# Kernel tuning notes

Hardware: AMD Instinct MI355X
Metric: run time of the kernel (lower is better)

Reference implementation:

```python
import jax, jax.numpy as jnp
import numpy as np

ROW, COL = 135, 240          # input_size / ratio
N = ROW * COL                # 32400 sampled pixels
MB = 2025                    # minibatch_size
NITER = N // MB              # 16
K = 9                        # feature_neibor_length
NC = 19                      # num_classes
FULL_ROW, FULL_COL = 1080, 1920
H, W, C = 270, 480, 512


def setup_inputs() -> dict:
    key = jax.random.key(0)
    k1, k2, k3, k4 = jax.random.split(key, 4)
    features_tensor = jax.random.normal(k1, (1, C, H, W), jnp.float32)
    outputs = jax.random.normal(k2, (1, NC, H, W), jnp.float32)
    classes_prototypes = jax.random.normal(k3, (1, NC, C), jnp.float32)
    # random.sample -> unique indices, then sorted (torch.sort on sampled ids)
    sample_index = jnp.sort(jax.random.permutation(k4, H * W)[:N]).astype(jnp.int32)
    return {"features_tensor": features_tensor, "outputs": outputs,
            "classes_prototypes": classes_prototypes, "sample_index": sample_index}


def reference(features_tensor, outputs, classes_prototypes, sample_index):
    b, c, h, w = features_tensor.shape
    # [1,C,H,W] -> [H*W,C], gather sampled pixels -> [N,C]
    feats = features_tensor[0].transpose(1, 2, 0).reshape(h * w, c)[sample_index]
    # predicted class per pixel (softmax is monotone -> argmax over class dim)
    cls = jnp.argmax(outputs[0].reshape(NC, h * w), axis=0)[sample_index]  # [N] int
    protos = classes_prototypes[0]                       # [NC, C]
    feats_sq = jnp.sum(feats * feats, axis=-1)           # [N]
    proto_sq = jnp.sum(protos * protos, axis=-1)         # [NC]

    def step(_, xs):
        mb_feats, mb_cls = xs                            # [MB,C], [MB]
        mb_sq = jnp.sum(mb_feats * mb_feats, axis=-1)    # [MB]
        # squared Euclidean distance, clamped (dim==3 branch: no sqrt)
        d = mb_sq[:, None] - 2.0 * (mb_feats @ feats.T) + feats_sq[None, :]
        d = jnp.maximum(d, 1e-12)                        # [MB, N]
        _, idx = jax.lax.top_k(-d, K)                    # K nearest -> [MB, K]
        nb_cls = cls[idx]                                # neighbor class ids [MB,K]
        counts = jnp.sum(jax.nn.one_hot(nb_cls, NC, dtype=jnp.float32), axis=1)  # [MB,NC]
        p = counts / float(K)
        ent = jnp.sum(-p * jnp.log(p + 1e-6), axis=1) / np.float32(np.log(NC))   # [MB]
        # disparity: rank of predicted class among prototypes sorted by distance
        dp = mb_sq[:, None] - 2.0 * (mb_feats @ protos.T) + proto_sq[None, :]
        dp = jnp.maximum(dp, 1e-12)                      # [MB, NC]
        order = jnp.argsort(dp, axis=1)                  # [MB, NC] class ids by distance
        rank = jnp.argmax(order == mb_cls[:, None], axis=1)  # [MB]
        score = rank.astype(jnp.float32) / float(NC - 1)
        return None, (ent, score)

    xs = (feats.reshape(NITER, MB, c), cls.reshape(NITER, MB))
    _, (ents, scores) = jax.lax.scan(step, None, xs)
    purity = ents.reshape(N)
    entropy = scores.reshape(N)
    full_p = jnp.zeros(FULL_ROW * FULL_COL, jnp.float32).at[sample_index].set(purity)
    full_e = jnp.zeros(FULL_ROW * FULL_COL, jnp.float32).at[sample_index].set(entropy)
    return (full_p.reshape(FULL_ROW, FULL_COL), full_e.reshape(FULL_ROW, FULL_COL))
```

## Files before the change

### kernel.cpp

```cpp
#include <hip/hip_runtime.h>
#include <math.h>

#define H_ 270
#define W_ 480
#define HW_ (H_ * W_)
#define C_ 512
#define NC_ 19
#define N_ 32400
#define NP_ 32512
#define FULLPIX 2073600
#define K_ 9

#define BM 64
#define BN 128
#define BK 16
#define TM 4
#define TN 8

static_assert(NP_ % BN == 0, "pad");
static_assert(NP_ % BM == 0, "pad");
static_assert(C_ % BK == 0, "pad");

__global__ void gather_kernel(const float* __restrict__ feat,
                              const int* __restrict__ sidx,
                              float* __restrict__ MT) {
    int i = blockIdx.x * 256 + threadIdx.x;
    int c = blockIdx.y;
    float v = 0.0f;
    if (i < N_) v = feat[(size_t)c * HW_ + sidx[i]];
    MT[(size_t)c * NP_ + i] = v;
}

__global__ void sq_kernel(const float* __restrict__ MT, float* __restrict__ fsq) {
    int i = blockIdx.x * 256 + threadIdx.x;
    float s = 0.0f;
    for (int c = 0; c < C_; ++c) {
        float v = MT[(size_t)c * NP_ + i];
        s = fmaf(v, v, s);
    }
    fsq[i] = (i < N_) ? s : 1e30f;
}

__global__ void cls_kernel(const float* __restrict__ outs,
                           const int* __restrict__ sidx,
                           int* __restrict__ cls) {
    int i = blockIdx.x * 256 + threadIdx.x;
    if (i >= NP_) return;
    if (i >= N_) { cls[i] = 0; return; }
    int p = sidx[i];
    float best = outs[p];
    int bk = 0;
#pragma unroll
    for (int k = 1; k < NC_; ++k) {
        float v = outs[(size_t)k * HW_ + p];
        if (v > best) { best = v; bk = k; }
    }
    cls[i] = bk;
}

__launch_bounds__(256, 2)
__global__ void knn_kernel(const float* __restrict__ MT,
                           const float* __restrict__ fsq,
                           const int* __restrict__ cls,
                           const int* __restrict__ sidx,
                           float* __restrict__ out) {
    __shared__ float As[BK][BM];
    __shared__ float Bs[BK][BN];
    __shared__ float dT[BN][BM + 4];

    const int tid = threadIdx.x;
    const int tx = tid & 15;
    const int ty = tid >> 4;
    const int ibase = blockIdx.x * BM;

    float t9d[K_];
    int   t9i[K_];
#pragma unroll
    for (int s = 0; s < K_; ++s) { t9d[s] = 1e38f; t9i[s] = -1; }
    float w9 = 1e38f;

    float si[TM];
#pragma unroll
    for (int m = 0; m < TM; ++m) si[m] = fsq[ibase + ty * TM + m];

    float acc[TM][TN];

    for (int jt = 0; jt < NP_ / BN; ++jt) {
        const int jbase = jt * BN;
#pragma unroll
        for (int m = 0; m < TM; ++m)
#pragma unroll
            for (int n = 0; n < TN; ++n) acc[m][n] = 0.0f;

        for (int ck = 0; ck < C_ / BK; ++ck) {
            const int cc = ck * BK;
            {
                int kk = tid >> 4, seg = tid & 15;
                *(float4*)&As[kk][seg * 4] =
                    *(const float4*)&MT[(size_t)(cc + kk) * NP_ + ibase + seg * 4];
            }
#pragma unroll
            for (int l = 0; l < 2; ++l) {
                int idx = tid + l * 256;
                int kk = idx >> 5, seg = idx & 31;
                *(float4*)&Bs[kk][seg * 4] =
                    *(const float4*)&MT[(size_t)(cc + kk) * NP_ + jbase + seg * 4];
            }
            __syncthreads();
#pragma unroll
            for (int kk = 0; kk < BK; ++kk) {
                float4 av  = *(const float4*)&As[kk][ty * TM];
                float4 bv0 = *(const float4*)&Bs[kk][tx * TN];
                float4 bv1 = *(const float4*)&Bs[kk][tx * TN + 4];
                float a[TM] = {av.x, av.y, av.z, av.w};
                float b[TN] = {bv0.x, bv0.y, bv0.z, bv0.w, bv1.x, bv1.y, bv1.z, bv1.w};
#pragma unroll
                for (int m = 0; m < TM; ++m)
#pragma unroll
                    for (int n = 0; n < TN; ++n)
                        acc[m][n] = fmaf(a[m], b[n], acc[m][n]);
            }
            __syncthreads();
        }

        float sj[TN];
#pragma unroll
        for (int n = 0; n < TN; ++n) sj[n] = fsq[jbase + tx * TN + n];
#pragma unroll
        for (int n = 0; n < TN; ++n) {
            float d0 = fmaxf(si[0] - 2.0f * acc[0][n] + sj[n], 1e-12f);
            float d1 = fmaxf(si[1] - 2.0f * acc[1][n] + sj[n], 1e-12f);
            float d2 = fmaxf(si[2] - 2.0f * acc[2][n] + sj[n], 1e-12f);
            float d3 = fmaxf(si[3] - 2.0f * acc[3][n] + sj[n], 1e-12f);
            *(float4*)&dT[tx * TN + n][ty * TM] = make_float4(d0, d1, d2, d3);
        }
        __syncthreads();

        if (tid < BM) {
            int jlim = min(BN, N_ - jbase);
#pragma unroll 4
            for (int jj = 0; jj < jlim; ++jj) {
                float d = dT[jj][tid];
                if (d < w9) {
                    float cd = d;
                    int   ci = jbase + jj;
#pragma unroll
                    for (int s = 0; s < K_; ++s) {
                        if (cd < t9d[s]) {
                            float td = t9d[s]; t9d[s] = cd; cd = td;
                            int   ti = t9i[s]; t9i[s] = ci; ci = ti;
                        }
                    }
                    w9 = t9d[K_ - 1];
                }
            }
        }
    }

    if (tid < BM) {
        int i = ibase + tid;
        if (i < N_) {
            int nb[K_];
#pragma unroll
            for (int s = 0; s < K_; ++s) nb[s] = cls[t9i[s]];
            float ent = 0.0f;
#pragma unroll
            for (int k = 0; k < NC_; ++k) {
                int c = 0;
#pragma unroll
                for (int s = 0; s < K_; ++s) c += (nb[s] == k) ? 1 : 0;
                if (c > 0) {
                    float p = (float)c / 9.0f;
                    ent += -p * logf(p + 1e-6f);
                }
            }
            ent = ent / 2.9444389791664403f;
            out[sidx[i]] = ent;
        }
    }
}

__global__ void proto_kernel(const float* __restrict__ MT,
                             const float* __restrict__ fsq,
                             const int* __restrict__ cls,
                             const int* __restrict__ sidx,
                             const float* __restrict__ protos,
                             float* __restrict__ out) {
    __shared__ float P[NC_][C_];
    __shared__ float psq[NC_];
    int tid = threadIdx.x;
    for (int idx = tid; idx < NC_ * C_; idx += 256)
        P[idx >> 9][idx & (C_ - 1)] = protos[idx];
    __syncthreads();
    if (tid < NC_) {
        float s = 0.0f;
        for (int c = 0; c < C_; ++c) { float v = P[tid][c]; s = fmaf(v, v, s); }
        psq[tid] = s;
    }
    __syncthreads();

    int i = blockIdx.x * 256 + tid;
    if (i >= N_) return;

    float accp[NC_];
#pragma unroll
    for (int k = 0; k < NC_; ++k) accp[k] = 0.0f;
    for (int c = 0; c < C_; ++c) {
        float f = MT[(size_t)c * NP_ + i];
#pragma unroll
        for (int k = 0; k < NC_; ++k) accp[k] = fmaf(f, P[k][c], accp[k]);
    }
    float s = fsq[i];
    int ci = cls[i];
    float dp[NC_];
    float dc = 0.0f;
#pragma unroll
    for (int k = 0; k < NC_; ++k) {
        float v = fmaxf(s - 2.0f * accp[k] + psq[k], 1e-12f);
        dp[k] = v;
        if (k == ci) dc = v;
    }
    int rank = 0;
#pragma unroll
    for (int k = 0; k < NC_; ++k) {
        rank += (dp[k] < dc) ? 1 : 0;
        rank += ((k < ci) && (dp[k] == dc)) ? 1 : 0;
    }
    out[FULLPIX + sidx[i]] = (float)rank / 18.0f;
}

extern "C" void kernel_launch(void* const* d_in, const int* in_sizes, int n_in,
                              void* d_out, int out_size, void* d_ws, size_t ws_size,
                              hipStream_t stream) {
    const float* feat   = (const float*)d_in[0];
    const float* outs   = (const float*)d_in[1];
    const float* protos = (const float*)d_in[2];
    const int*   sidx   = (const int*)d_in[3];
    float* out = (float*)d_out;

    char* ws = (char*)d_ws;
    float* MT  = (float*)ws;
    float* fsq = (float*)(ws + (size_t)66584576);
    int*   cls = (int*)(ws + (size_t)66584576 + 130048);

    hipMemsetAsync(d_out, 0, (size_t)2 * FULLPIX * sizeof(float), stream);

    gather_kernel<<<dim3(NP_ / 256, C_), 256, 0, stream>>>(feat, sidx, MT);
    sq_kernel<<<NP_ / 256, 256, 0, stream>>>(MT, fsq);
    cls_kernel<<<NP_ / 256, 256, 0, stream>>>(outs, sidx, cls);
    knn_kernel<<<NP_ / BM, 256, 0, stream>>>(MT, fsq, cls, sidx, out);
    proto_kernel<<<NP_ / 256, 256, 0, stream>>>(MT, fsq, cls, sidx, protos, out);
}
```

Measured before the change: 23.31 ms.

## Split KNN column range across blocks, distribute top-k selection, double-buffer GEMM tiles

Splits the candidate dimension into four parts so that four times as many blocks run, and adds a finalize kernel that merges the per-part top-9 lists and computes the entropy. Every thread now keeps its own top-9 for two rows across 16 columns, and the lists are merged through shared memory. Before, only 64 threads per block did the serial insertion. The GEMM loop gains register-staged double buffering and XOR-swizzled B tiles to cut bank conflicts. The row norm and the clamp are dropped from the comparison because they do not change the ordering. The cost is extra workspace traffic for the partial results, more registers per thread, and tie-breaking by index that may differ slightly from top_k.

```diff
diff --git a/kernel.cpp b/kernel.cpp
--- a/kernel.cpp
+++ b/kernel.cpp
@@ -14,8 +14,10 @@
 #define BM 64
 #define BN 128
 #define BK 16
-#define TM 4
-#define TN 8
+#define NTILES (NP_ / BN)
+#define CKS (C_ / BK)
+#define JSPLIT 4
+#define TILES_PER_PART 64
 
 static_assert(NP_ % BN == 0, "pad");
 static_assert(NP_ % BM == 0, "pad");
@@ -58,126 +60,207 @@
     cls[i] = bk;
 }
 
-__launch_bounds__(256, 2)
+union SmU {
+    struct { float As[2][BK][BM]; float Bs[2][BK * BN]; } st;
+    struct { float md[BM][73]; int mi[BM][73]; } mg;
+};
+
+#define FMA4(bv, n0)                                                        \
+    acc[0][(n0) + 0] = fmaf(av.x, (bv).x, acc[0][(n0) + 0]);                \
+    acc[1][(n0) + 0] = fmaf(av.y, (bv).x, acc[1][(n0) + 0]);                \
+    acc[0][(n0) + 1] = fmaf(av.x, (bv).y, acc[0][(n0) + 1]);                \
+    acc[1][(n0) + 1] = fmaf(av.y, (bv).y, acc[1][(n0) + 1]);                \
+    acc[0][(n0) + 2] = fmaf(av.x, (bv).z, acc[0][(n0) + 2]);                \
+    acc[1][(n0) + 2] = fmaf(av.y, (bv).z, acc[1][(n0) + 2]);                \
+    acc[0][(n0) + 3] = fmaf(av.x, (bv).w, acc[0][(n0) + 3]);                \
+    acc[1][(n0) + 3] = fmaf(av.y, (bv).w, acc[1][(n0) + 3]);
+
+__launch_bounds__(256, 3)
 __global__ void knn_kernel(const float* __restrict__ MT,
                            const float* __restrict__ fsq,
-                           const int* __restrict__ cls,
-                           const int* __restrict__ sidx,
-                           float* __restrict__ out) {
-    __shared__ float As[BK][BM];
-    __shared__ float Bs[BK][BN];
-    __shared__ float dT[BN][BM + 4];
-
-    const int tid = threadIdx.x;
-    const int tx = tid & 15;
-    const int ty = tid >> 4;
-    const int ibase = blockIdx.x * BM;
-
-    float t9d[K_];
-    int   t9i[K_];
-#pragma unroll
-    for (int s = 0; s < K_; ++s) { t9d[s] = 1e38f; t9i[s] = -1; }
-    float w9 = 1e38f;
-
-    float si[TM];
-#pragma unroll
-    for (int m = 0; m < TM; ++m) si[m] = fsq[ibase + ty * TM + m];
-
-    float acc[TM][TN];
-
-    for (int jt = 0; jt < NP_ / BN; ++jt) {
+                           float* __restrict__ wd, int* __restrict__ wi) {
+    __shared__ SmU sm;
+
+    const int tid  = threadIdx.x;
+    const int tx   = tid & 7;
+    const int ty   = tid >> 3;
+    const int part = blockIdx.x / 508;
+    const int rowb = blockIdx.x % 508;
+    const int ibase = rowb * BM;
+
+    const int t0 = part * TILES_PER_PART;
+    const int t1 = min(t0 + TILES_PER_PART, NTILES);
+
+    const int akk  = tid >> 4;
+    const int aseg = tid & 15;
+    const int bkk0 = tid >> 5;
+    const int bsg0 = tid & 31;
+    const int bkk1 = (tid + 256) >> 5;
+    const int bsg1 = bsg0;
+    const int bpc0 = (bsg0 * 4) ^ (((bsg0 >> 3) & 3) << 2);
+    const int bpc1 = bpc0;
+
+    const int xv   = ((tx >> 1) & 3) << 2;
+    const int bcol = tx * 16;
+
+    float t9d[2][K_];
+    int   t9i[2][K_];
+#pragma unroll
+    for (int m = 0; m < 2; ++m)
+#pragma unroll
+        for (int s = 0; s < K_; ++s) { t9d[m][s] = 1e38f; t9i[m][s] = 0x7fffffff; }
+    float w90 = 1e38f, w91 = 1e38f;
+
+    for (int jt = t0; jt < t1; ++jt) {
         const int jbase = jt * BN;
-#pragma unroll
-        for (int m = 0; m < TM; ++m)
-#pragma unroll
-            for (int n = 0; n < TN; ++n) acc[m][n] = 0.0f;
-
-        for (int ck = 0; ck < C_ / BK; ++ck) {
-            const int cc = ck * BK;
-            {
-                int kk = tid >> 4, seg = tid & 15;
-                *(float4*)&As[kk][seg * 4] =
-                    *(const float4*)&MT[(size_t)(cc + kk) * NP_ + ibase + seg * 4];
-            }
-#pragma unroll
-            for (int l = 0; l < 2; ++l) {
-                int idx = tid + l * 256;
-                int kk = idx >> 5, seg = idx & 31;
-                *(float4*)&Bs[kk][seg * 4] =
-                    *(const float4*)&MT[(size_t)(cc + kk) * NP_ + jbase + seg * 4];
+        float acc[2][16];
+#pragma unroll
+        for (int n = 0; n < 16; ++n) { acc[0][n] = 0.0f; acc[1][n] = 0.0f; }
+
+        *(float4*)&sm.st.As[0][akk][aseg * 4] =
+            *(const float4*)&MT[(size_t)akk * NP_ + ibase + aseg * 4];
+        *(float4*)&sm.st.Bs[0][bkk0 * BN + bpc0] =
+            *(const float4*)&MT[(size_t)bkk0 * NP_ + jbase + bsg0 * 4];
+        *(float4*)&sm.st.Bs[0][bkk1 * BN + bpc1] =
+            *(const float4*)&MT[(size_t)bkk1 * NP_ + jbase + bsg1 * 4];
+        __syncthreads();
+
+        int cur = 0;
+        for (int ck = 0; ck < CKS; ++ck) {
+            float4 ra, rb0, rb1;
+            if (ck + 1 < CKS) {
+                const int cc = (ck + 1) * BK;
+                ra  = *(const float4*)&MT[(size_t)(cc + akk)  * NP_ + ibase + aseg * 4];
+                rb0 = *(const float4*)&MT[(size_t)(cc + bkk0) * NP_ + jbase + bsg0 * 4];
+                rb1 = *(const float4*)&MT[(size_t)(cc + bkk1) * NP_ + jbase + bsg1 * 4];
+            }
+#pragma unroll
+            for (int kk = 0; kk < BK; ++kk) {
+                float2 av = *(const float2*)&sm.st.As[cur][kk][ty * 2];
+                const float* bb = &sm.st.Bs[cur][kk * BN];
+                float4 b0 = *(const float4*)&bb[(bcol + 0)  ^ xv];
+                float4 b1 = *(const float4*)&bb[(bcol + 4)  ^ xv];
+                float4 b2 = *(const float4*)&bb[(bcol + 8)  ^ xv];
+                float4 b3 = *(const float4*)&bb[(bcol + 12) ^ xv];
+                FMA4(b0, 0) FMA4(b1, 4) FMA4(b2, 8) FMA4(b3, 12)
+            }
+            if (ck + 1 < CKS) {
+                const int nxt = cur ^ 1;
+                *(float4*)&sm.st.As[nxt][akk][aseg * 4] = ra;
+                *(float4*)&sm.st.Bs[nxt][bkk0 * BN + bpc0] = rb0;
+                *(float4*)&sm.st.Bs[nxt][bkk1 * BN + bpc1] = rb1;
             }
             __syncthreads();
-#pragma unroll
-            for (int kk = 0; kk < BK; ++kk) {
-                float4 av  = *(const float4*)&As[kk][ty * TM];
-                float4 bv0 = *(const float4*)&Bs[kk][tx * TN];
-                float4 bv1 = *(const float4*)&Bs[kk][tx * TN + 4];
-                float a[TM] = {av.x, av.y, av.z, av.w};
-                float b[TN] = {bv0.x, bv0.y, bv0.z, bv0.w, bv1.x, bv1.y, bv1.z, bv1.w};
-#pragma unroll
-                for (int m = 0; m < TM; ++m)
-#pragma unroll
-                    for (int n = 0; n < TN; ++n)
-                        acc[m][n] = fmaf(a[m], b[n], acc[m][n]);
-            }
-            __syncthreads();
-        }
-
-        float sj[TN];
-#pragma unroll
-        for (int n = 0; n < TN; ++n) sj[n] = fsq[jbase + tx * TN + n];
-#pragma unroll
-        for (int n = 0; n < TN; ++n) {
-            float d0 = fmaxf(si[0] - 2.0f * acc[0][n] + sj[n], 1e-12f);
-            float d1 = fmaxf(si[1] - 2.0f * acc[1][n] + sj[n], 1e-12f);
-            float d2 = fmaxf(si[2] - 2.0f * acc[2][n] + sj[n], 1e-12f);
-            float d3 = fmaxf(si[3] - 2.0f * acc[3][n] + sj[n], 1e-12f);
-            *(float4*)&dT[tx * TN + n][ty * TM] = make_float4(d0, d1, d2, d3);
-        }
-        __syncthreads();
-
-        if (tid < BM) {
-            int jlim = min(BN, N_ - jbase);
-#pragma unroll 4
-            for (int jj = 0; jj < jlim; ++jj) {
-                float d = dT[jj][tid];
-                if (d < w9) {
-                    float cd = d;
-                    int   ci = jbase + jj;
-#pragma unroll
-                    for (int s = 0; s < K_; ++s) {
-                        if (cd < t9d[s]) {
-                            float td = t9d[s]; t9d[s] = cd; cd = td;
-                            int   ti = t9i[s]; t9i[s] = ci; ci = ti;
-                        }
-                    }
-                    w9 = t9d[K_ - 1];
+            cur ^= 1;
+        }
+
+        float4 s0 = *(const float4*)&fsq[jbase + bcol + 0];
+        float4 s1 = *(const float4*)&fsq[jbase + bcol + 4];
+        float4 s2 = *(const float4*)&fsq[jbase + bcol + 8];
+        float4 s3 = *(const float4*)&fsq[jbase + bcol + 12];
+        float sj[16] = {s0.x, s0.y, s0.z, s0.w, s1.x, s1.y, s1.z, s1.w,
+                        s2.x, s2.y, s2.z, s2.w, s3.x, s3.y, s3.z, s3.w};
+        const int cb = jbase + bcol;
+#pragma unroll
+        for (int n = 0; n < 16; ++n) {
+            float d0 = fmaf(-2.0f, acc[0][n], sj[n]);
+            if (d0 < w90) {
+                float cd = d0; int ci = cb + n;
+#pragma unroll
+                for (int s = 0; s < K_; ++s) {
+                    bool sw = cd < t9d[0][s];
+                    float td = t9d[0][s]; int ti = t9i[0][s];
+                    t9d[0][s] = sw ? cd : td; t9i[0][s] = sw ? ci : ti;
+                    cd = sw ? td : cd; ci = sw ? ti : ci;
                 }
-            }
-        }
-    }
-
+                w90 = t9d[0][K_ - 1];
+            }
+            float d1 = fmaf(-2.0f, acc[1][n], sj[n]);
+            if (d1 < w91) {
+                float cd = d1; int ci = cb + n;
+#pragma unroll
+                for (int s = 0; s < K_; ++s) {
+                    bool sw = cd < t9d[1][s];
+                    float td = t9d[1][s]; int ti = t9i[1][s];
+                    t9d[1][s] = sw ? cd : td; t9i[1][s] = sw ? ci : ti;
+                    cd = sw ? td : cd; ci = sw ? ti : ci;
+                }
+                w91 = t9d[1][K_ - 1];
+            }
+        }
+    }
+
+#pragma unroll
+    for (int m = 0; m < 2; ++m) {
+        const int r = ty * 2 + m;
+#pragma unroll
+        for (int s = 0; s < K_; ++s) {
+            sm.mg.md[r][tx * K_ + s] = t9d[m][s];
+            sm.mg.mi[r][tx * K_ + s] = t9i[m][s];
+        }
+    }
+    __syncthreads();
     if (tid < BM) {
-        int i = ibase + tid;
-        if (i < N_) {
-            int nb[K_];
-#pragma unroll
-            for (int s = 0; s < K_; ++s) nb[s] = cls[t9i[s]];
-            float ent = 0.0f;
-#pragma unroll
-            for (int k = 0; k < NC_; ++k) {
-                int c = 0;
-#pragma unroll
-                for (int s = 0; s < K_; ++s) c += (nb[s] == k) ? 1 : 0;
-                if (c > 0) {
-                    float p = (float)c / 9.0f;
-                    ent += -p * logf(p + 1e-6f);
-                }
-            }
-            ent = ent / 2.9444389791664403f;
-            out[sidx[i]] = ent;
-        }
-    }
+        const int r = tid;
+        float bd[K_]; int bx[K_];
+#pragma unroll
+        for (int s = 0; s < K_; ++s) { bd[s] = 1e38f; bx[s] = 0x7fffffff; }
+        for (int e = 0; e < 8 * K_; ++e) {
+            float cd = sm.mg.md[r][e];
+            int   ci = sm.mg.mi[r][e];
+#pragma unroll
+            for (int s = 0; s < K_; ++s) {
+                bool sw = (cd < bd[s]) || (cd == bd[s] && ci < bx[s]);
+                float td = bd[s]; int ti = bx[s];
+                bd[s] = sw ? cd : td; bx[s] = sw ? ci : ti;
+                cd = sw ? td : cd; ci = sw ? ti : ci;
+            }
+        }
+#pragma unroll
+        for (int s = 0; s < K_; ++s) {
+            wd[(size_t)(part * K_ + s) * NP_ + ibase + r] = bd[s];
+            wi[(size_t)(part * K_ + s) * NP_ + ibase + r] = bx[s];
+        }
+    }
+}
+
+__global__ void finalize_kernel(const float* __restrict__ wd, const int* __restrict__ wi,
+                                const int* __restrict__ cls, const int* __restrict__ sidx,
+                                float* __restrict__ out) {
+    int i = blockIdx.x * 256 + threadIdx.x;
+    if (i >= N_) return;
+    float bd[K_]; int bx[K_];
+#pragma unroll
+    for (int s = 0; s < K_; ++s) { bd[s] = 1e38f; bx[s] = 0x7fffffff; }
+#pragma unroll
+    for (int p = 0; p < JSPLIT; ++p)
+#pragma unroll
+        for (int s = 0; s < K_; ++s) {
+            float cd = wd[(size_t)(p * K_ + s) * NP_ + i];
+            int   ci = wi[(size_t)(p * K_ + s) * NP_ + i];
+#pragma unroll
+            for (int t = 0; t < K_; ++t) {
+                bool sw = (cd < bd[t]) || (cd == bd[t] && ci < bx[t]);
+                float td = bd[t]; int ti = bx[t];
+                bd[t] = sw ? cd : td; bx[t] = sw ? ci : ti;
+                cd = sw ? td : cd; ci = sw ? ti : ci;
+            }
+        }
+    int nb[K_];
+#pragma unroll
+    for (int s = 0; s < K_; ++s) nb[s] = cls[bx[s]];
+    float ent = 0.0f;
+#pragma unroll
+    for (int k = 0; k < NC_; ++k) {
+        int c = 0;
+#pragma unroll
+        for (int s = 0; s < K_; ++s) c += (nb[s] == k) ? 1 : 0;
+        if (c > 0) {
+            float p = (float)c / 9.0f;
+            ent += -p * logf(p + 1e-6f);
+        }
+    }
+    out[sidx[i]] = ent / 2.9444389791664403f;
 }
 
 __global__ void proto_kernel(const float* __restrict__ MT,
@@ -240,14 +323,17 @@
 
     char* ws = (char*)d_ws;
     float* MT  = (float*)ws;
-    float* fsq = (float*)(ws + (size_t)66584576);
-    int*   cls = (int*)(ws + (size_t)66584576 + 130048);
+    float* fsq = (float*)(ws + 66584576ull);
+    int*   cls = (int*)  (ws + 66584576ull + 130048ull);
+    float* wd  = (float*)(ws + 66844672ull);
+    int*   wi  = (int*)  (ws + 71526400ull);
 
     hipMemsetAsync(d_out, 0, (size_t)2 * FULLPIX * sizeof(float), stream);
 
     gather_kernel<<<dim3(NP_ / 256, C_), 256, 0, stream>>>(feat, sidx, MT);
     sq_kernel<<<NP_ / 256, 256, 0, stream>>>(MT, fsq);
     cls_kernel<<<NP_ / 256, 256, 0, stream>>>(outs, sidx, cls);
-    knn_kernel<<<NP_ / BM, 256, 0, stream>>>(MT, fsq, cls, sidx, out);
+    knn_kernel<<<508 * JSPLIT, 256, 0, stream>>>(MT, fsq, wd, wi);
+    finalize_kernel<<<(N_ + 255) / 256, 256, 0, stream>>>(wd, wi, cls, sidx, out);
     proto_kernel<<<NP_ / 256, 256, 0, stream>>>(MT, fsq, cls, sidx, protos, out);
 }
```

Result: slower. 31.30 ms (+34.3%).
